# Optimization experiments

Hardware: AMD Instinct MI355X
Metric: run time of the kernel (lower is better)

Reference implementation:

```python
import jax, jax.numpy as jnp
import numpy as np

ETA = 0.01
EPSILON = 1e-08


def setup_inputs() -> dict:
    key = jax.random.key(0)
    k1, k2 = jax.random.split(key)
    B, N = 2000000, 16  # batch (time steps), num_assets
    weights = jax.random.uniform(k1, (B, N), dtype=jnp.float32)
    next_returns = jax.random.normal(k2, (B, N), dtype=jnp.float32) * 0.02
    return {"weights": weights, "next_returns": next_returns}


def reference(weights, next_returns):
    # portfolio return per time step: (B,)
    R = jnp.sum(weights * next_returns, axis=1)
    batch_size = R.shape[0]
    eta = jnp.asarray(ETA, R.dtype)
    eps = jnp.asarray(EPSILON, R.dtype)

    def step(carry, R_t):
        A_prev, B_prev = carry
        delta_A = eta * (R_t - A_prev)
        delta_B = eta * (R_t * R_t - B_prev)
        variance = jnp.maximum(B_prev - A_prev * A_prev, eps)
        denom = variance ** 1.5
        D_t = (B_prev * delta_A - 0.5 * A_prev * delta_B) / denom
        return (A_prev + delta_A, B_prev + delta_B), D_t

    init = (jnp.asarray(0.0, R.dtype), jnp.asarray(EPSILON, R.dtype))
    _, D = jax.lax.scan(step, init, R)
    return -jnp.sum(D) / batch_size
```

## Files before the change

kernel.cpp:

```cpp
#include <hip/hip_runtime.h>


#define D_ETA 0.01
#define D_C   (1.0 - D_ETA)
#define D_EPS 1e-8

constexpr int BLOCK = 256;
constexpr int CHUNK = 2048;
constexpr int LPT   = CHUNK / BLOCK;
constexpr int PASSES = CHUNK / 64;
constexpr int BATCH  = 8;

__device__ __forceinline__ void block_scan(double& m, double& sA, double& sB,
                                           double* mS, double* aS, double* bS) {
    int tid = threadIdx.x;
    mS[tid] = m; aS[tid] = sA; bS[tid] = sB;
    __syncthreads();
#pragma unroll
    for (int off = 1; off < BLOCK; off <<= 1) {
        double pm = 1.0, pa = 0.0, pb = 0.0;
        if (tid >= off) { pm = mS[tid - off]; pa = aS[tid - off]; pb = bS[tid - off]; }
        __syncthreads();
        if (tid >= off) {
            sA = m * pa + sA;
            sB = m * pb + sB;
            m  = pm * m;
        }
        mS[tid] = m; aS[tid] = sA; bS[tid] = sB;
        __syncthreads();
    }
}

__global__ __launch_bounds__(BLOCK, 4) void k1_fused(
    const float* __restrict__ w, const float* __restrict__ x, int nrows,
    float* __restrict__ Rws,
    double* __restrict__ blkM, double* __restrict__ blkA, double* __restrict__ blkB)
{
    __shared__ float  Rlds[CHUNK];
    __shared__ double mS[BLOCK], aS[BLOCK], bS[BLOCK];

    const int tid = threadIdx.x;
    const int b   = blockIdx.x;
    const long long base = (long long)b * CHUNK;
    const int q    = tid & 3;
    const int rsub = tid >> 2;
    const float4* w4 = (const float4*)w;
    const float4* x4 = (const float4*)x;

    const bool full = (base + CHUNK <= (long long)nrows);

    if (full) {
        const long long f0 = base * 4 + tid;
        for (int p0 = 0; p0 < PASSES; p0 += BATCH) {
            float4 av[BATCH], bv[BATCH];
#pragma unroll
            for (int u = 0; u < BATCH; ++u) {
                const long long f = f0 + (long long)(p0 + u) * 256;
                av[u] = w4[f];
                bv[u] = x4[f];
            }
            __builtin_amdgcn_sched_barrier(0);
#pragma unroll
            for (int u = 0; u < BATCH; ++u) {
                double p = (double)av[u].x * bv[u].x
                         + (double)av[u].y * bv[u].y
                         + (double)av[u].z * bv[u].z
                         + (double)av[u].w * bv[u].w;
                p += __shfl_xor(p, 1, 64);
                p += __shfl_xor(p, 2, 64);
                if (q == 0) Rlds[(p0 + u) * 64 + rsub] = (float)p;
            }
        }
    } else {
        for (int p = 0; p < PASSES; ++p) {
            long long row = base + (long long)p * 64 + rsub;
            double pd = 0.0;
            if (row < (long long)nrows) {
                long long f = row * 4 + q;
                float4 a = w4[f], c = x4[f];
                pd = (double)a.x * c.x + (double)a.y * c.y
                   + (double)a.z * c.z + (double)a.w * c.w;
            }
            pd += __shfl_xor(pd, 1, 64);
            pd += __shfl_xor(pd, 2, 64);
            if (q == 0) Rlds[p * 64 + rsub] = (float)pd;
        }
    }
    __syncthreads();

    float rv[LPT];
    {
        const float4* Rp = (const float4*)&Rlds[tid * LPT];
        float4 u0 = Rp[0], u1 = Rp[1];
        rv[0] = u0.x; rv[1] = u0.y; rv[2] = u0.z; rv[3] = u0.w;
        rv[4] = u1.x; rv[5] = u1.y; rv[6] = u1.z; rv[7] = u1.w;
    }
    long long g0 = base + (long long)tid * LPT;
    long long rem = (long long)nrows - g0;
    int len = rem >= LPT ? LPT : (rem > 0 ? (int)rem : 0);

    if (len == LPT) {
        float4* Rp = (float4*)(Rws + g0);
        Rp[0] = make_float4(rv[0], rv[1], rv[2], rv[3]);
        Rp[1] = make_float4(rv[4], rv[5], rv[6], rv[7]);
    } else {
        for (int k = 0; k < len; ++k) Rws[g0 + k] = rv[k];
    }

    double m = 1.0, sA = 0.0, sB = 0.0;
    for (int k = 0; k < len; ++k) {
        double r = (double)rv[k];
        sA = D_C * sA + D_ETA * r;
        sB = D_C * sB + D_ETA * (r * r);
        m *= D_C;
    }
    block_scan(m, sA, sB, mS, aS, bS);
    if (tid == BLOCK - 1) {
        blkM[b] = m;
        blkA[b] = sA;
        blkB[b] = sB;
    }
}

__device__ __forceinline__ float row_R(const float* __restrict__ w,
                                       const float* __restrict__ x,
                                       long long row) {
    const float4* w4 = (const float4*)(w + row * 16);
    const float4* x4 = (const float4*)(x + row * 16);
    double r = 0.0;
#pragma unroll
    for (int q = 0; q < 4; ++q) {
        float4 a = w4[q];
        float4 b = x4[q];
        r += (double)a.x * (double)b.x;
        r += (double)a.y * (double)b.y;
        r += (double)a.z * (double)b.z;
        r += (double)a.w * (double)b.w;
    }
    return (float)r;
}

__device__ __forceinline__ int load_seg(const float* __restrict__ Rws,
                                        const float* __restrict__ w,
                                        const float* __restrict__ x,
                                        long long g0, int nrows, float* rv) {
    long long rem = (long long)nrows - g0;
    int len = rem >= LPT ? LPT : (rem > 0 ? (int)rem : 0);
    if (Rws) {
        if (len == LPT) {
            const float4* Rp = (const float4*)(Rws + g0);
            float4 u = Rp[0], v = Rp[1];
            rv[0]=u.x; rv[1]=u.y; rv[2]=u.z; rv[3]=u.w;
            rv[4]=v.x; rv[5]=v.y; rv[6]=v.z; rv[7]=v.w;
        } else {
            for (int k = 0; k < len; ++k) rv[k] = Rws[g0 + k];
        }
    } else {
        for (int k = 0; k < len; ++k) rv[k] = row_R(w, x, g0 + k);
    }
    return len;
}

__global__ __launch_bounds__(BLOCK) void k2_partials(
    const float* __restrict__ Rws,
    const float* __restrict__ w, const float* __restrict__ x, int nrows,
    double* __restrict__ blkM, double* __restrict__ blkA, double* __restrict__ blkB)
{
    __shared__ double mS[BLOCK], aS[BLOCK], bS[BLOCK];
    int tid = threadIdx.x;
    long long g0 = (long long)blockIdx.x * CHUNK + (long long)tid * LPT;
    float rv[LPT];
    int len = load_seg(Rws, w, x, g0, nrows, rv);

    double m = 1.0, sA = 0.0, sB = 0.0;
    for (int k = 0; k < len; ++k) {
        double r = (double)rv[k];
        sA = D_C * sA + D_ETA * r;
        sB = D_C * sB + D_ETA * (r * r);
        m *= D_C;
    }
    block_scan(m, sA, sB, mS, aS, bS);
    if (tid == BLOCK - 1) {
        blkM[blockIdx.x] = m;
        blkA[blockIdx.x] = sA;
        blkB[blockIdx.x] = sB;
    }
}

__global__ __launch_bounds__(BLOCK) void k3_scan(
    int nb,
    const double* __restrict__ blkM, const double* __restrict__ blkA,
    const double* __restrict__ blkB,
    double* __restrict__ A0, double* __restrict__ B0)
{
    __shared__ double mS[BLOCK], aS[BLOCK], bS[BLOCK];
    int tid = threadIdx.x;
    int K = (nb + BLOCK - 1) / BLOCK;
    int g0 = tid * K;
    int g1 = g0 + K; if (g1 > nb) g1 = nb;

    double m = 1.0, sA = 0.0, sB = 0.0;
    for (int g = g0; g < g1; ++g) {
        double mg = blkM[g], ag = blkA[g], bg = blkB[g];
        sA = mg * sA + ag;
        sB = mg * sB + bg;
        m *= mg;
    }
    block_scan(m, sA, sB, mS, aS, bS);

    double em = 1.0, ea = 0.0, eb = 0.0;
    if (tid > 0) { em = mS[tid - 1]; ea = aS[tid - 1]; eb = bS[tid - 1]; }
    double A = ea;
    double B = em * D_EPS + eb;
    for (int g = g0; g < g1; ++g) {
        A0[g] = A; B0[g] = B;
        double mg = blkM[g], ag = blkA[g], bg = blkB[g];
        A = mg * A + ag;
        B = mg * B + bg;
    }
}

__global__ __launch_bounds__(BLOCK) void k4_dsum(
    const float* __restrict__ Rws,
    const float* __restrict__ w, const float* __restrict__ x, int nrows,
    const double* __restrict__ A0, const double* __restrict__ B0,
    double* __restrict__ bsum)
{
    __shared__ double mS[BLOCK], aS[BLOCK], bS[BLOCK];
    __shared__ double wsum[BLOCK / 64];
    int tid = threadIdx.x;
    long long g0 = (long long)blockIdx.x * CHUNK + (long long)tid * LPT;
    float rv[LPT];
    int len = load_seg(Rws, w, x, g0, nrows, rv);

    double m = 1.0, sA = 0.0, sB = 0.0;
    for (int k = 0; k < len; ++k) {
        double r = (double)rv[k];
        sA = D_C * sA + D_ETA * r;
        sB = D_C * sB + D_ETA * (r * r);
        m *= D_C;
    }
    block_scan(m, sA, sB, mS, aS, bS);

    double em = 1.0, ea = 0.0, eb = 0.0;
    if (tid > 0) { em = mS[tid - 1]; ea = aS[tid - 1]; eb = bS[tid - 1]; }
    double A = em * A0[blockIdx.x] + ea;
    double B = em * B0[blockIdx.x] + eb;

    double dsum = 0.0;
    for (int k = 0; k < len; ++k) {
        double r = (double)rv[k];
        double dA = D_ETA * (r - A);
        double dB = D_ETA * (r * r - B);
        double var = B - A * A;
        if (var < D_EPS) var = D_EPS;
        double denom = var * sqrt(var);
        dsum += (B * dA - 0.5 * A * dB) / denom;
        A += dA;
        B += dB;
    }

#pragma unroll
    for (int off = 32; off > 0; off >>= 1) dsum += __shfl_down(dsum, off, 64);
    if ((tid & 63) == 0) wsum[tid >> 6] = dsum;
    __syncthreads();
    if (tid == 0) bsum[blockIdx.x] = wsum[0] + wsum[1] + wsum[2] + wsum[3];
}

__global__ __launch_bounds__(BLOCK) void k5_final(
    const double* __restrict__ bsum, int nb, int nrows, float* __restrict__ out)
{
    __shared__ double sh[BLOCK / 64];
    int tid = threadIdx.x;
    double s = 0.0;
    for (int i = tid; i < nb; i += BLOCK) s += bsum[i];
#pragma unroll
    for (int off = 32; off > 0; off >>= 1) s += __shfl_down(s, off, 64);
    if ((tid & 63) == 0) sh[tid >> 6] = s;
    __syncthreads();
    if (tid == 0) out[0] = (float)(-(sh[0] + sh[1] + sh[2] + sh[3]) / (double)nrows);
}

extern "C" void kernel_launch(void* const* d_in, const int* in_sizes, int n_in,
                              void* d_out, int out_size, void* d_ws, size_t ws_size,
                              hipStream_t stream)
{
    const float* w = (const float*)d_in[0];
    const float* x = (const float*)d_in[1];
    int nrows = in_sizes[0] / 16;
    int nb  = (nrows + CHUNK - 1) / CHUNK;

    char* ws = (char*)d_ws;
    double* blkM = (double*)(ws + 64);
    double* blkA = blkM + nb;
    double* blkB = blkA + nb;
    double* A0   = blkB + nb;
    double* B0   = A0 + nb;
    double* bsum = B0 + nb;

    size_t off = 64 + (size_t)6 * nb * sizeof(double);
    off = (off + 255) & ~(size_t)255;
    float* Rws = nullptr;
    if (ws_size >= off + (size_t)nrows * sizeof(float))
        Rws = (float*)(ws + off);

    if (Rws) {
        k1_fused<<<nb, BLOCK, 0, stream>>>(w, x, nrows, Rws, blkM, blkA, blkB);
    } else {
        k2_partials<<<nb, BLOCK, 0, stream>>>(Rws, w, x, nrows, blkM, blkA, blkB);
    }
    k3_scan<<<1, BLOCK, 0, stream>>>(nb, blkM, blkA, blkB, A0, B0);
    k4_dsum<<<nb, BLOCK, 0, stream>>>(Rws, w, x, nrows, A0, B0, bsum);
    k5_final<<<1, BLOCK, 0, stream>>>(bsum, nb, nrows, (float*)d_out);
}
```

Baseline: 286.8 us.

## Halve chunk size, software-pipeline loads, and replace shuffle reduction with LDS partials

Shrinks the per-block chunk from 2048 to 1024 rows, so each thread now scans 4 rows instead of 8 and twice as many blocks are launched. The batched load loop becomes a rolling three-deep prefetch pipeline. Each lane now writes its quarter-row double partial into a 4xCHUNK shared array, and the cross-lane shuffle reduction is dropped. The partials are summed when rows are gathered per thread. The row dot-product helper is also split into four independent partial sums to shorten the dependency chain, at the cost of more LDS (32KB) and more block-level carry entries to combine.

```diff
diff --git a/kernel.cpp b/kernel.cpp
--- a/kernel.cpp
+++ b/kernel.cpp
@@ -5,11 +5,10 @@
 #define D_C   (1.0 - D_ETA)
 #define D_EPS 1e-8
 
-constexpr int BLOCK = 256;
-constexpr int CHUNK = 2048;
-constexpr int LPT   = CHUNK / BLOCK;
+constexpr int BLOCK  = 256;
+constexpr int CHUNK  = 1024;
+constexpr int LPT    = CHUNK / BLOCK;
 constexpr int PASSES = CHUNK / 64;
-constexpr int BATCH  = 8;
 
 __device__ __forceinline__ void block_scan(double& m, double& sA, double& sB,
                                            double* mS, double* aS, double* bS) {
@@ -36,7 +35,7 @@
     float* __restrict__ Rws,
     double* __restrict__ blkM, double* __restrict__ blkA, double* __restrict__ blkB)
 {
-    __shared__ float  Rlds[CHUNK];
+    __shared__ double Qs[4][CHUNK];
     __shared__ double mS[BLOCK], aS[BLOCK], bS[BLOCK];
 
     const int tid = threadIdx.x;
@@ -51,58 +50,57 @@
 
     if (full) {
         const long long f0 = base * 4 + tid;
-        for (int p0 = 0; p0 < PASSES; p0 += BATCH) {
-            float4 av[BATCH], bv[BATCH];
-#pragma unroll
-            for (int u = 0; u < BATCH; ++u) {
-                const long long f = f0 + (long long)(p0 + u) * 256;
-                av[u] = w4[f];
-                bv[u] = x4[f];
+        float4 a0 = w4[f0];
+        float4 c0 = x4[f0];
+        float4 a1 = w4[f0 + 256];
+        float4 c1 = x4[f0 + 256];
+        float4 a2 = w4[f0 + 512];
+        float4 c2 = x4[f0 + 512];
+#pragma unroll
+        for (int p = 0; p < PASSES; ++p) {
+            float4 a3 = make_float4(0.f, 0.f, 0.f, 0.f);
+            float4 c3 = make_float4(0.f, 0.f, 0.f, 0.f);
+            if (p + 3 < PASSES) {
+                a3 = w4[f0 + (long long)(p + 3) * 256];
+                c3 = x4[f0 + (long long)(p + 3) * 256];
             }
             __builtin_amdgcn_sched_barrier(0);
-#pragma unroll
-            for (int u = 0; u < BATCH; ++u) {
-                double p = (double)av[u].x * bv[u].x
-                         + (double)av[u].y * bv[u].y
-                         + (double)av[u].z * bv[u].z
-                         + (double)av[u].w * bv[u].w;
-                p += __shfl_xor(p, 1, 64);
-                p += __shfl_xor(p, 2, 64);
-                if (q == 0) Rlds[(p0 + u) * 64 + rsub] = (float)p;
-            }
+            double d = (double)a0.x * c0.x + (double)a0.y * c0.y
+                     + (double)a0.z * c0.z + (double)a0.w * c0.w;
+            Qs[q][p * 64 + rsub] = d;
+            a0 = a1; c0 = c1;
+            a1 = a2; c1 = c2;
+            a2 = a3; c2 = c3;
         }
     } else {
         for (int p = 0; p < PASSES; ++p) {
             long long row = base + (long long)p * 64 + rsub;
-            double pd = 0.0;
             if (row < (long long)nrows) {
                 long long f = row * 4 + q;
                 float4 a = w4[f], c = x4[f];
-                pd = (double)a.x * c.x + (double)a.y * c.y
-                   + (double)a.z * c.z + (double)a.w * c.w;
+                Qs[q][p * 64 + rsub] =
+                      (double)a.x * c.x + (double)a.y * c.y
+                    + (double)a.z * c.z + (double)a.w * c.w;
             }
-            pd += __shfl_xor(pd, 1, 64);
-            pd += __shfl_xor(pd, 2, 64);
-            if (q == 0) Rlds[p * 64 + rsub] = (float)pd;
         }
     }
     __syncthreads();
 
-    float rv[LPT];
-    {
-        const float4* Rp = (const float4*)&Rlds[tid * LPT];
-        float4 u0 = Rp[0], u1 = Rp[1];
-        rv[0] = u0.x; rv[1] = u0.y; rv[2] = u0.z; rv[3] = u0.w;
-        rv[4] = u1.x; rv[5] = u1.y; rv[6] = u1.z; rv[7] = u1.w;
-    }
     long long g0 = base + (long long)tid * LPT;
     long long rem = (long long)nrows - g0;
     int len = rem >= LPT ? LPT : (rem > 0 ? (int)rem : 0);
 
+    float rv[LPT];
+#pragma unroll
+    for (int r = 0; r < LPT; ++r) {
+        int lr = tid * LPT + r;
+        double d01 = Qs[0][lr] + Qs[1][lr];
+        double d23 = Qs[2][lr] + Qs[3][lr];
+        rv[r] = (float)(d01 + d23);
+    }
+
     if (len == LPT) {
-        float4* Rp = (float4*)(Rws + g0);
-        Rp[0] = make_float4(rv[0], rv[1], rv[2], rv[3]);
-        Rp[1] = make_float4(rv[4], rv[5], rv[6], rv[7]);
+        *(float4*)(Rws + g0) = make_float4(rv[0], rv[1], rv[2], rv[3]);
     } else {
         for (int k = 0; k < len; ++k) Rws[g0 + k] = rv[k];
     }
@@ -127,17 +125,28 @@
                                        long long row) {
     const float4* w4 = (const float4*)(w + row * 16);
     const float4* x4 = (const float4*)(x + row * 16);
-    double r = 0.0;
-#pragma unroll
-    for (int q = 0; q < 4; ++q) {
-        float4 a = w4[q];
-        float4 b = x4[q];
-        r += (double)a.x * (double)b.x;
-        r += (double)a.y * (double)b.y;
-        r += (double)a.z * (double)b.z;
-        r += (double)a.w * (double)b.w;
-    }
-    return (float)r;
+    double d0 = 0.0, d1 = 0.0, d2 = 0.0, d3 = 0.0;
+    {
+        float4 a = w4[0], b = x4[0];
+        d0 = (double)a.x * b.x + (double)a.y * b.y
+           + (double)a.z * b.z + (double)a.w * b.w;
+    }
+    {
+        float4 a = w4[1], b = x4[1];
+        d1 = (double)a.x * b.x + (double)a.y * b.y
+           + (double)a.z * b.z + (double)a.w * b.w;
+    }
+    {
+        float4 a = w4[2], b = x4[2];
+        d2 = (double)a.x * b.x + (double)a.y * b.y
+           + (double)a.z * b.z + (double)a.w * b.w;
+    }
+    {
+        float4 a = w4[3], b = x4[3];
+        d3 = (double)a.x * b.x + (double)a.y * b.y
+           + (double)a.z * b.z + (double)a.w * b.w;
+    }
+    return (float)((d0 + d1) + (d2 + d3));
 }
 
 __device__ __forceinline__ int load_seg(const float* __restrict__ Rws,
@@ -148,10 +157,8 @@
     int len = rem >= LPT ? LPT : (rem > 0 ? (int)rem : 0);
     if (Rws) {
         if (len == LPT) {
-            const float4* Rp = (const float4*)(Rws + g0);
-            float4 u = Rp[0], v = Rp[1];
-            rv[0]=u.x; rv[1]=u.y; rv[2]=u.z; rv[3]=u.w;
-            rv[4]=v.x; rv[5]=v.y; rv[6]=v.z; rv[7]=v.w;
+            float4 u = *(const float4*)(Rws + g0);
+            rv[0] = u.x; rv[1] = u.y; rv[2] = u.z; rv[3] = u.w;
         } else {
             for (int k = 0; k < len; ++k) rv[k] = Rws[g0 + k];
         }
```

Measured after the change: 289.1 us. About the same (+0.8%).
